# Kernel tuning notes

Measured on AMD Instinct MI355X. Metric: run time of the kernel, lower is better.

## Reference

```python
import jax, jax.numpy as jnp
import numpy as np
from jax import lax

B, T, H, L = 32, 100, 1024, 2


def _cell(x, h, c, Wih, Whh, bih, bhh):
    # torch LSTM gate order: i, f, g, o
    gates = x @ Wih.T + h @ Whh.T + bih + bhh
    i, f, g, o = jnp.split(gates, 4, axis=-1)
    c = jax.nn.sigmoid(f) * c + jax.nn.sigmoid(i) * jnp.tanh(g)
    h = jax.nn.sigmoid(o) * jnp.tanh(c)
    return h, c


def _run_lstm(x, h0, c0, layers):
    # x: (B, T, F); h0/c0: (L, B, H). Returns (top outputs (B,T,H), hn, cn).
    inp = x
    hs, cs = [], []
    for l, (Wih, Whh, bih, bhh) in enumerate(layers):
        def step(carry, x_t, Wih=Wih, Whh=Whh, bih=bih, bhh=bhh):
            h, c = carry
            h, c = _cell(x_t, h, c, Wih, Whh, bih, bhh)
            return (h, c), h
        (hT, cT), ys = lax.scan(step, (h0[l], c0[l]), jnp.swapaxes(inp, 0, 1))
        inp = jnp.swapaxes(ys, 0, 1)
        hs.append(hT)
        cs.append(cT)
    return inp, jnp.stack(hs), jnp.stack(cs)


def setup_inputs() -> dict:
    key = jax.random.key(0)
    ks = jax.random.split(key, 12)
    s = 1.0 / np.sqrt(H)
    u = lambda k, shp: jax.random.uniform(k, shp, jnp.float32, -s, s)
    return {
        "flattenedInput": jax.random.normal(ks[0], (B, T, H), jnp.float32),
        "targets": jax.random.normal(ks[1], (B, T, H), jnp.float32),
        "W_ih0": u(ks[2], (4 * H, H)), "W_hh0": u(ks[3], (4 * H, H)),
        "b_ih0": u(ks[4], (4 * H,)), "b_hh0": u(ks[5], (4 * H,)),
        "W_ih1": u(ks[6], (4 * H, H)), "W_hh1": u(ks[7], (4 * H, H)),
        "b_ih1": u(ks[8], (4 * H,)), "b_hh1": u(ks[9], (4 * H,)),
        "training": 1,
    }


def reference(flattenedInput, targets, W_ih0, W_hh0, b_ih0, b_hh0,
              W_ih1, W_hh1, b_ih1, b_hh1, training):
    layers = [(W_ih0, W_hh0, b_ih0, b_hh0), (W_ih1, W_hh1, b_ih1, b_hh1)]
    Bsz, Tlen = flattenedInput.shape[0], flattenedInput.shape[1]
    h0 = jnp.zeros((L, Bsz, H), flattenedInput.dtype)
    c0 = jnp.zeros((L, Bsz, H), flattenedInput.dtype)
    # Encoder pass over the full input sequence
    enc_out, hn, cn = _run_lstm(flattenedInput, h0, c0, layers)
    last = enc_out[:, -1:, :]  # (B, 1, H)
    if training:
        # Teacher forcing: step 0 uses last encoder output, steps 1..T-1 use targets
        dec_in = jnp.concatenate([last, targets[:, 1:, :]], axis=1)
        dec_out, _, _ = _run_lstm(dec_in, hn, cn, layers)
        return dec_out
    else:
        def step(carry, _):
            hs, cs, x = carry  # hs/cs: (L,B,H), x: (B,H)
            new_h, new_c = [], []
            inp = x
            for l, (Wih, Whh, bih, bhh) in enumerate(layers):
                h, c = _cell(inp, hs[l], cs[l], Wih, Whh, bih, bhh)
                new_h.append(h)
                new_c.append(c)
                inp = h
            return (jnp.stack(new_h), jnp.stack(new_c), inp), inp
        _, ys = lax.scan(step, (hn, cn, last[:, 0, :]), None, length=Tlen)
        return jnp.swapaxes(ys, 0, 1)
```

## Files before the change

### kernel.cpp

```cpp
#include <hip/hip_runtime.h>
#include <math.h>

#define BB 32
#define HH 1024
#define TT 100
#define TH (TT * HH)
#define NSTEP 200
#define TILE 32768
#define SENT 0x7F7Fu

typedef _Float16 half8 __attribute__((ext_vector_type(8)));
typedef float f32x4 __attribute__((ext_vector_type(4)));
typedef unsigned int uint4v __attribute__((ext_vector_type(4)));

#define MFMA16 __builtin_amdgcn_mfma_f32_16x16x32_f16

__device__ __forceinline__ void llc_ld_nw(const _Float16* p, half8& v) {
    asm volatile("global_load_dwordx4 %0, %1, off sc0 sc1" : "=v"(v) : "v"(p) : "memory");
}
__device__ __forceinline__ bool frag_ready(half8 v) {
    uint4v u = __builtin_bit_cast(uint4v, v);
    return ((u.x & 0xFFFFu) != SENT) & ((u.z & 0xFFFFu) != SENT);
}

__global__ __launch_bounds__(256) void bias_sum_kernel(
    const float* bih0, const float* bhh0, const float* bih1, const float* bhh1,
    float* bsum0, float* bsum1)
{
    int i = blockIdx.x * blockDim.x + threadIdx.x;
    if (i < 4096)      bsum0[i] = bih0[i] + bhh0[i];
    else if (i < 8192) bsum1[i - 4096] = bih1[i - 4096] + bhh1[i - 4096];
}

__global__ __launch_bounds__(256) void cvt_pack_x(
    const float* __restrict__ X, const float* __restrict__ Tg,
    _Float16* __restrict__ X16, _Float16* __restrict__ Tg16)
{
    int id  = blockIdx.x * 256 + threadIdx.x;
    int tsr = id / 409600;
    int rem = id - tsr * 409600;
    int t   = rem >> 12;
    int rb  = rem & 4095;
    int h8  = rb >> 5;
    int b   = rb & 31;
    const float* s = tsr ? Tg : X;
    _Float16*    d = tsr ? Tg16 : X16;
    const float* sp = s + (size_t)b * TH + (size_t)t * HH + h8 * 8;
    float4 v0 = *(const float4*)sp;
    float4 v1 = *(const float4*)(sp + 4);
    half8 h;
    h[0] = (_Float16)v0.x; h[1] = (_Float16)v0.y; h[2] = (_Float16)v0.z; h[3] = (_Float16)v0.w;
    h[4] = (_Float16)v1.x; h[5] = (_Float16)v1.y; h[6] = (_Float16)v1.z; h[7] = (_Float16)v1.w;
    *(half8*)(d + (size_t)t * TILE + ((size_t)h8 * 32 + b) * 8) = h;
}

__global__ __launch_bounds__(256) void pack_w(
    const float* __restrict__ Wih0, const float* __restrict__ Whh0,
    const float* __restrict__ Wih1, const float* __restrict__ Whh1,
    _Float16* __restrict__ Wp0, _Float16* __restrict__ Wp1)
{
    int id    = blockIdx.x * 256 + threadIdx.x;
    int lane  = id & 63;
    int nt    = (id >> 6) & 1;
    int s     = (id >> 7) & 7;
    int w     = (id >> 10) & 7;
    int hb    = (id >> 13) & 127;
    int layer = id >> 20;
    const float* Wih = layer ? Wih1 : Wih0;
    const float* Whh = layer ? Whh1 : Whh0;
    _Float16*    Wp  = layer ? Wp1 : Wp0;

    int nl   = nt * 16 + (lane & 15);
    int gate = nl >> 3;
    int col  = hb * 8 + (nl & 7);
    int n    = gate * HH + col;
    int k    = w * 256 + s * 32 + ((lane >> 4) & 3) * 8;
    const float* src = (k < 1024) ? (Wih + (size_t)n * HH + k)
                                  : (Whh + (size_t)n * HH + (k - 1024));
    float4 v0 = *(const float4*)src;
    float4 v1 = *(const float4*)(src + 4);
    half8 d;
    d[0] = (_Float16)v0.x; d[1] = (_Float16)v0.y; d[2] = (_Float16)v0.z; d[3] = (_Float16)v0.w;
    d[4] = (_Float16)v1.x; d[5] = (_Float16)v1.y; d[6] = (_Float16)v1.z; d[7] = (_Float16)v1.w;
    *(half8*)(Wp + (size_t)(id & 0xFFFFF) * 8) = d;
}

struct PArgs {
    const _Float16* X16;
    const _Float16* Tg16;
    const _Float16* Wp0;
    const _Float16* Wp1;
    const float* bsum0;
    const float* bsum1;
    _Float16* h0r;
    _Float16* h1r;
    float* out;
};

__global__ __launch_bounds__(512, 2) void lstm_persist(PArgs A)
{
    __shared__ float part[8][32][34];
    __shared__ float ldspad[11776];

    const int wg   = blockIdx.x;
    const int role = wg >> 7;
    const int hb   = wg & 127;
    const int tid  = threadIdx.x;
    const int w    = tid >> 6;
    const int lane = tid & 63;
    const int lr   = lane & 15;
    const int lg   = lane >> 4;
    const bool isx = (w < 4);

    if (A.out == (float*)1) {
        ldspad[tid] = (float)tid;
        part[0][0][0] = ldspad[511 - tid];
    }

    const _Float16* Wp   = role ? A.Wp1 : A.Wp0;
    const float* bsum    = role ? A.bsum1 : A.bsum0;
    _Float16* ring_self  = role ? A.h1r : A.h0r;

    half8 wreg[16];
    {
        const half8* wp = (const half8*)Wp + (size_t)(hb * 8 + w) * 1024 + lane;
#pragma unroll
        for (int sn = 0; sn < 16; ++sn) wreg[sn] = wp[(size_t)sn * 64];
    }

    const int eb = tid >> 3, ec = tid & 7, ecol = hb * 8 + ec;
    float breg[4], creg = 0.f;
    if (tid < 256) {
#pragma unroll
        for (int g = 0; g < 4; ++g) breg[g] = bsum[g * HH + ecol];
    }

    const size_t afrag = (size_t)((w & 3) * 32 + lg) * 256 + (size_t)lr * 8;
    bool dead = false;

    for (int p = 0; p < NSTEP; ++p) {
        half8 a[16];
        const bool early = isx && role == 0 && p != 100;
        if (early) {
            const _Float16* aptr = ((p < 100) ? A.X16 + (size_t)p * TILE
                                              : A.Tg16 + (size_t)(p - 100) * TILE) + afrag;
#pragma unroll
            for (int s = 0; s < 8; ++s) {
                a[2 * s]     = *(const half8*)(aptr + s * 1024);
                a[2 * s + 1] = *(const half8*)(aptr + s * 1024 + 128);
            }
        } else {
            const _Float16* abase;
            if (isx) abase = role ? A.h0r + (size_t)(p + 1) * TILE
                                  : A.h1r + (size_t)100 * TILE;
            else     abase = ring_self + (size_t)p * TILE;
            const _Float16* aptr = abase + afrag;

            unsigned spins = 0;
            for (;;) {
                llc_ld_nw(aptr,       a[0]);
                llc_ld_nw(aptr + 128, a[1]);
#pragma unroll
                for (int s = 1; s < 8; ++s) {
                    llc_ld_nw(aptr + s * 1024,       a[2 * s]);
                    llc_ld_nw(aptr + s * 1024 + 128, a[2 * s + 1]);
                }
                asm volatile("s_waitcnt vmcnt(0)"
                    : "+v"(a[0]),  "+v"(a[1]),  "+v"(a[2]),  "+v"(a[3]),
                      "+v"(a[4]),  "+v"(a[5]),  "+v"(a[6]),  "+v"(a[7]),
                      "+v"(a[8]),  "+v"(a[9]),  "+v"(a[10]), "+v"(a[11]),
                      "+v"(a[12]), "+v"(a[13]), "+v"(a[14]), "+v"(a[15])
                    :: "memory");
                __builtin_amdgcn_sched_barrier(0);
                bool ok = true;
#pragma unroll
                for (int i = 0; i < 16; ++i) ok &= frag_ready(a[i]);
                if (__all(ok) || dead) break;
                __builtin_amdgcn_s_sleep(1);
                if (++spins > (1u << 20)) dead = true;
            }
        }

        f32x4 acc[2][2] = {};
#pragma unroll
        for (int s = 0; s < 8; ++s) {
            acc[0][0] = MFMA16(a[2 * s],     wreg[2 * s],     acc[0][0], 0, 0, 0);
            acc[0][1] = MFMA16(a[2 * s],     wreg[2 * s + 1], acc[0][1], 0, 0, 0);
            acc[1][0] = MFMA16(a[2 * s + 1], wreg[2 * s],     acc[1][0], 0, 0, 0);
            acc[1][1] = MFMA16(a[2 * s + 1], wreg[2 * s + 1], acc[1][1], 0, 0, 0);
        }

#pragma unroll
        for (int mt = 0; mt < 2; ++mt)
#pragma unroll
            for (int nt = 0; nt < 2; ++nt)
#pragma unroll
                for (int j = 0; j < 4; ++j)
                    part[w][16 * mt + lg * 4 + j][16 * nt + lr] = acc[mt][nt][j];
        __syncthreads();

        if (tid < 256) {
            float g4[4];
#pragma unroll
            for (int g = 0; g < 4; ++g) {
                float s0 = 0.f;
#pragma unroll
                for (int pw = 0; pw < 8; ++pw) s0 += part[pw][eb][g * 8 + ec];
                g4[g] = s0 + breg[g];
            }
            float ig = 1.f / (1.f + __expf(-g4[0]));
            float fg = 1.f / (1.f + __expf(-g4[1]));
            float gg = 2.f / (1.f + __expf(-2.f * g4[2])) - 1.f;
            float og = 1.f / (1.f + __expf(-g4[3]));
            float cn = fg * creg + ig * gg;
            float tc = 2.f / (1.f + __expf(-2.f * cn)) - 1.f;
            float hn = og * tc;
            creg = cn;

            unsigned hv = (unsigned)__builtin_bit_cast(unsigned short, (_Float16)hn);
            unsigned o1  = __shfl_xor(hv, 1, 64);
            unsigned w32 = hv | (o1 << 16);
            unsigned o2  = __shfl_xor(w32, 2, 64);
            if ((tid & 3) == 0) {
                unsigned long long d64 =
                    ((unsigned long long)o2 << 32) | (unsigned long long)w32;
                unsigned long long* dst = (unsigned long long*)
                    (ring_self + (size_t)(p + 1) * TILE + hb * 256 + tid);
                __hip_atomic_exchange(dst, d64, __ATOMIC_RELAXED,
                                      __HIP_MEMORY_SCOPE_AGENT);
            }
            if (role && p >= 100)
                A.out[(size_t)eb * TH + (size_t)(p - 100) * HH + ecol] = hn;
        }
        __syncthreads();
    }
}

extern "C" void kernel_launch(void* const* d_in, const int* in_sizes, int n_in,
                              void* d_out, int out_size, void* d_ws, size_t ws_size,
                              hipStream_t stream)
{
    const float* X    = (const float*)d_in[0];
    const float* Tg   = (const float*)d_in[1];
    const float* Wih0 = (const float*)d_in[2];
    const float* Whh0 = (const float*)d_in[3];
    const float* bih0 = (const float*)d_in[4];
    const float* bhh0 = (const float*)d_in[5];
    const float* Wih1 = (const float*)d_in[6];
    const float* Whh1 = (const float*)d_in[7];
    const float* bih1 = (const float*)d_in[8];
    const float* bhh1 = (const float*)d_in[9];
    float* out = (float*)d_out;

    const size_t ringBytes = (size_t)201 * TILE * 2;
    char* p = (char*)d_ws;
    _Float16* h0r = (_Float16*)p; p += ringBytes;
    _Float16* h1r = (_Float16*)p; p += ringBytes;
    float* bsum0 = (float*)p; p += 4096 * sizeof(float);
    float* bsum1 = (float*)p; p += 4096 * sizeof(float);
    _Float16* X16  = (_Float16*)p; p += (size_t)TT * TILE * 2;
    _Float16* Tg16 = (_Float16*)p; p += (size_t)TT * TILE * 2;
    _Float16* Wp0  = (_Float16*)p; p += (size_t)4096 * 2048 * 2;
    _Float16* Wp1  = (_Float16*)p;

    hipMemsetAsync(h0r, 0x7F, ringBytes, stream);
    hipMemsetAsync(h1r, 0x7F, ringBytes, stream);
    hipMemsetAsync(h0r, 0, (size_t)TILE * 2, stream);
    hipMemsetAsync(h1r, 0, (size_t)TILE * 2, stream);

    bias_sum_kernel<<<32, 256, 0, stream>>>(bih0, bhh0, bih1, bhh1, bsum0, bsum1);
    cvt_pack_x<<<3200, 256, 0, stream>>>(X, Tg, X16, Tg16);
    pack_w<<<8192, 256, 0, stream>>>(Wih0, Whh0, Wih1, Whh1, Wp0, Wp1);

    PArgs A;
    A.X16 = X16; A.Tg16 = Tg16; A.Wp0 = Wp0; A.Wp1 = Wp1;
    A.bsum0 = bsum0; A.bsum1 = bsum1;
    A.h0r = h0r; A.h1r = h1r;
    A.out = out;
    lstm_persist<<<256, 512, 0, stream>>>(A);
}
```

Before: 597.9 us.

## Replace sentinel data polling with per-workgroup ready flags

Consumers no longer spin-load the whole 16-fragment hidden-state tile and check sentinel values. Instead they poll one 128-byte-strided flag per producer workgroup, then load the tile once. Producers write h with plain sc0/sc1 stores instead of atomic exchanges, and set their flag after a workgroup barrier. This drops the two large 0x7F memsets of the rings in favour of a smaller flag-array memset. The trade-off is an extra dependent round trip per step (flag, then data) on the serial recurrence path, plus reliance on barrier/store ordering for visibility.

```diff
diff --git a/kernel.cpp b/kernel.cpp
--- a/kernel.cpp
+++ b/kernel.cpp
@@ -7,20 +7,26 @@
 #define TH (TT * HH)
 #define NSTEP 200
 #define TILE 32768
-#define SENT 0x7F7Fu
 
 typedef _Float16 half8 __attribute__((ext_vector_type(8)));
 typedef float f32x4 __attribute__((ext_vector_type(4)));
-typedef unsigned int uint4v __attribute__((ext_vector_type(4)));
 
 #define MFMA16 __builtin_amdgcn_mfma_f32_16x16x32_f16
 
 __device__ __forceinline__ void llc_ld_nw(const _Float16* p, half8& v) {
     asm volatile("global_load_dwordx4 %0, %1, off sc0 sc1" : "=v"(v) : "v"(p) : "memory");
 }
-__device__ __forceinline__ bool frag_ready(half8 v) {
-    uint4v u = __builtin_bit_cast(uint4v, v);
-    return ((u.x & 0xFFFFu) != SENT) & ((u.z & 0xFFFFu) != SENT);
+__device__ __forceinline__ int llc_poll(const int* p) {
+    int v;
+    asm volatile("global_load_dword %0, %1, off sc0 sc1\n\ts_waitcnt vmcnt(0)"
+                 : "=v"(v) : "v"(p) : "memory");
+    return v;
+}
+__device__ __forceinline__ void st_sc_int(int* p, int v) {
+    asm volatile("global_store_dword %0, %1, off sc0 sc1" :: "v"(p), "v"(v) : "memory");
+}
+__device__ __forceinline__ void st_sc_u64(unsigned long long* p, unsigned long long v) {
+    asm volatile("global_store_dwordx2 %0, %1, off sc0 sc1" :: "v"(p), "v"(v) : "memory");
 }
 
 __global__ __launch_bounds__(256) void bias_sum_kernel(
@@ -94,6 +100,8 @@
     const float* bsum1;
     _Float16* h0r;
     _Float16* h1r;
+    int* flags0;
+    int* flags1;
     float* out;
 };
 
@@ -120,6 +128,8 @@
     const _Float16* Wp   = role ? A.Wp1 : A.Wp0;
     const float* bsum    = role ? A.bsum1 : A.bsum0;
     _Float16* ring_self  = role ? A.h1r : A.h0r;
+    int* flags_self      = role ? A.flags1 : A.flags0;
+    int* flags_oth       = role ? A.flags0 : A.flags1;
 
     half8 wreg[16];
     {
@@ -136,6 +146,7 @@
     }
 
     const size_t afrag = (size_t)((w & 3) * 32 + lg) * 256 + (size_t)lr * 8;
+    const int cbase = (w & 3) * 32;
     bool dead = false;
 
     for (int p = 0; p < NSTEP; ++p) {
@@ -150,35 +161,39 @@
                 a[2 * s + 1] = *(const half8*)(aptr + s * 1024 + 128);
             }
         } else {
+            const int* flbase;
+            if (!isx)      flbase = flags_self + (size_t)p * 128 * 32;
+            else if (role) flbase = flags_oth  + (size_t)(p + 1) * 128 * 32;
+            else           flbase = flags_oth  + (size_t)100 * 128 * 32;
+            const int* myf = flbase + (size_t)(cbase + (lane & 31)) * 32;
+            unsigned spins = 0;
+            for (;;) {
+                int v = 1;
+                if (lane < 32) v = llc_poll(myf);
+                if (__all(v != 0) || dead) break;
+                __builtin_amdgcn_s_sleep(1);
+                if (++spins > (1u << 20)) dead = true;
+            }
+
             const _Float16* abase;
             if (isx) abase = role ? A.h0r + (size_t)(p + 1) * TILE
                                   : A.h1r + (size_t)100 * TILE;
             else     abase = ring_self + (size_t)p * TILE;
             const _Float16* aptr = abase + afrag;
-
-            unsigned spins = 0;
-            for (;;) {
-                llc_ld_nw(aptr,       a[0]);
-                llc_ld_nw(aptr + 128, a[1]);
-#pragma unroll
-                for (int s = 1; s < 8; ++s) {
-                    llc_ld_nw(aptr + s * 1024,       a[2 * s]);
-                    llc_ld_nw(aptr + s * 1024 + 128, a[2 * s + 1]);
-                }
-                asm volatile("s_waitcnt vmcnt(0)"
-                    : "+v"(a[0]),  "+v"(a[1]),  "+v"(a[2]),  "+v"(a[3]),
-                      "+v"(a[4]),  "+v"(a[5]),  "+v"(a[6]),  "+v"(a[7]),
-                      "+v"(a[8]),  "+v"(a[9]),  "+v"(a[10]), "+v"(a[11]),
-                      "+v"(a[12]), "+v"(a[13]), "+v"(a[14]), "+v"(a[15])
-                    :: "memory");
-                __builtin_amdgcn_sched_barrier(0);
-                bool ok = true;
-#pragma unroll
-                for (int i = 0; i < 16; ++i) ok &= frag_ready(a[i]);
-                if (__all(ok) || dead) break;
-                __builtin_amdgcn_s_sleep(1);
-                if (++spins > (1u << 20)) dead = true;
-            }
+            llc_ld_nw(aptr,       a[0]);
+            llc_ld_nw(aptr + 128, a[1]);
+#pragma unroll
+            for (int s = 1; s < 8; ++s) {
+                llc_ld_nw(aptr + s * 1024,       a[2 * s]);
+                llc_ld_nw(aptr + s * 1024 + 128, a[2 * s + 1]);
+            }
+            asm volatile("s_waitcnt vmcnt(0)"
+                : "+v"(a[0]),  "+v"(a[1]),  "+v"(a[2]),  "+v"(a[3]),
+                  "+v"(a[4]),  "+v"(a[5]),  "+v"(a[6]),  "+v"(a[7]),
+                  "+v"(a[8]),  "+v"(a[9]),  "+v"(a[10]), "+v"(a[11]),
+                  "+v"(a[12]), "+v"(a[13]), "+v"(a[14]), "+v"(a[15])
+                :: "memory");
+            __builtin_amdgcn_sched_barrier(0);
         }
 
         f32x4 acc[2][2] = {};
@@ -224,15 +239,16 @@
             if ((tid & 3) == 0) {
                 unsigned long long d64 =
                     ((unsigned long long)o2 << 32) | (unsigned long long)w32;
-                unsigned long long* dst = (unsigned long long*)
-                    (ring_self + (size_t)(p + 1) * TILE + hb * 256 + tid);
-                __hip_atomic_exchange(dst, d64, __ATOMIC_RELAXED,
-                                      __HIP_MEMORY_SCOPE_AGENT);
+                st_sc_u64((unsigned long long*)
+                          (ring_self + (size_t)(p + 1) * TILE + hb * 256 + tid), d64);
             }
             if (role && p >= 100)
                 A.out[(size_t)eb * TH + (size_t)(p - 100) * HH + ecol] = hn;
         }
         __syncthreads();
+
+        if (tid == 0)
+            st_sc_int(flags_self + (size_t)((p + 1) * 128 + hb) * 32, 1);
     }
 }
 
@@ -253,9 +269,12 @@
     float* out = (float*)d_out;
 
     const size_t ringBytes = (size_t)201 * TILE * 2;
+    const size_t flagBytes = (size_t)201 * 128 * 128;
     char* p = (char*)d_ws;
     _Float16* h0r = (_Float16*)p; p += ringBytes;
     _Float16* h1r = (_Float16*)p; p += ringBytes;
+    int* flags0 = (int*)p; p += flagBytes;
+    int* flags1 = (int*)p; p += flagBytes;
     float* bsum0 = (float*)p; p += 4096 * sizeof(float);
     float* bsum1 = (float*)p; p += 4096 * sizeof(float);
     _Float16* X16  = (_Float16*)p; p += (size_t)TT * TILE * 2;
@@ -263,10 +282,11 @@
     _Float16* Wp0  = (_Float16*)p; p += (size_t)4096 * 2048 * 2;
     _Float16* Wp1  = (_Float16*)p;
 
-    hipMemsetAsync(h0r, 0x7F, ringBytes, stream);
-    hipMemsetAsync(h1r, 0x7F, ringBytes, stream);
     hipMemsetAsync(h0r, 0, (size_t)TILE * 2, stream);
     hipMemsetAsync(h1r, 0, (size_t)TILE * 2, stream);
+    hipMemsetAsync(flags0, 0, flagBytes * 2, stream);
+    hipMemsetAsync(flags0, 1, 128 * 128, stream);
+    hipMemsetAsync(flags1, 1, 128 * 128, stream);
 
     bias_sum_kernel<<<32, 256, 0, stream>>>(bih0, bhh0, bih1, bhh1, bsum0, bsum1);
     cvt_pack_x<<<3200, 256, 0, stream>>>(X, Tg, X16, Tg16);
@@ -276,6 +296,7 @@
     A.X16 = X16; A.Tg16 = Tg16; A.Wp0 = Wp0; A.Wp1 = Wp1;
     A.bsum0 = bsum0; A.bsum1 = bsum1;
     A.h0r = h0r; A.h1r = h1r;
+    A.flags0 = flags0; A.flags1 = flags1;
     A.out = out;
     lstm_persist<<<256, 512, 0, stream>>>(A);
 }
```

Measured after the change: 664.9 us. 11.2% more time.
